# Kernel optimization log

Hardware: AMD Instinct MI355X
Metric: run time of the kernel (lower is better)

The kernel has to match this reference:

```python
import jax, jax.numpy as jnp
import numpy as np

N, M, D, H, T = 8192, 8192, 64, 32, 8
KERNEL_SCALE = 1.0


def setup_inputs() -> dict:
    key = jax.random.key(0)
    ks = jax.random.split(key, 8)
    s1 = 1.0 / np.sqrt(D)
    s2 = 1.0 / np.sqrt(H)
    return {
        "X": jax.random.normal(ks[0], (N, D), jnp.float32),
        "Y": jax.random.normal(ks[1], (M, D), jnp.float32),
        "Y_target": jax.random.normal(ks[2], (M, T), jnp.float32),
        "W1": jax.random.normal(ks[3], (D, H), jnp.float32) * s1,
        "b1": jnp.zeros((H,), jnp.float32),
        "W2": jax.random.normal(ks[4], (H, H), jnp.float32) * s2,
        "b2": jnp.zeros((H,), jnp.float32),
        "W3": jax.random.normal(ks[5], (H, H), jnp.float32) * s2,
        "b3": jnp.zeros((H,), jnp.float32),
    }


def _mlp(x, W1, b1, W2, b2, W3, b3):
    h = jax.nn.relu(x @ W1 + b1)
    h = jax.nn.relu(h @ W2 + b2)
    return jax.nn.relu(h @ W3 + b3)


def reference(X, Y, Y_target, W1, b1, W2, b2, W3, b3):
    Xf = _mlp(X, W1, b1, W2, b2, W3, b3)  # [N, H]
    Yf = _mlp(Y, W1, b1, W2, b2, W3, b3)  # [M, H]
    sq = (
        jnp.sum(Xf * Xf, axis=1, keepdims=True)
        + jnp.sum(Yf * Yf, axis=1)[None, :]
        - 2.0 * (Xf @ Yf.T)
    )
    sq = jnp.maximum(sq, 0.0)  # guard tiny negatives from cancellation
    kernel = jnp.exp(-sq / (2.0 * KERNEL_SCALE**2))  # [N, M]
    weights = kernel / jnp.sum(kernel, axis=1, keepdims=True)
    return weights @ Y_target  # [N, T]
```

## Files before the change

### kernel.cpp

```cpp
#include <hip/hip_runtime.h>
#include <hip/hip_bf16.h>
#include <cstddef>

#define N_ROWS 8192
#define M_ROWS 8192
#define D_IN   64
#define H_DIM  32
#define T_OUT  8
#define FDIM   48

#define NSPLIT   32
#define JSLICE   (M_ROWS / NSPLIT)
#define JTILE    32
#define NTILES   (JSLICE / JTILE)
#define LOG2E    1.4426950408889634f
#define NHALF_SC (-0.72134752044448169f)

typedef _Float16 half8  __attribute__((ext_vector_type(8)));
typedef _Float16 half4v __attribute__((ext_vector_type(4)));
typedef __fp16   fp16x2 __attribute__((ext_vector_type(2)));
typedef float    f32x16 __attribute__((ext_vector_type(16)));

__device__ __forceinline__ half8 ld_h8(const _Float16* p) {
    return *(const half8*)p;
}


__global__ __launch_bounds__(256) void feat_kernel(
    const float* __restrict__ X, const float* __restrict__ Y,
    const float* __restrict__ W1, const float* __restrict__ b1,
    const float* __restrict__ W2, const float* __restrict__ b2,
    const float* __restrict__ W3, const float* __restrict__ b3,
    _Float16* __restrict__ fh, _Float16* __restrict__ fl)
{
    __shared__ float xs [32 * 65];
    __shared__ float w1l[64 * 36];
    __shared__ float w2l[32 * 36];
    __shared__ float w3l[32 * 36];
    __shared__ float h1t[32 * 33];
    __shared__ float h2t[32 * 33];
    __shared__ float psums[8 * 32];
    __shared__ float bl[96];

    const int tid = threadIdx.x;
    const int rowbase = blockIdx.x * 32;
    const bool isX = rowbase < N_ROWS;
    const float* src = isX ? (X + (size_t)rowbase * D_IN)
                           : (Y + (size_t)(rowbase - N_ROWS) * D_IN);

    {
        const float4* g4 = (const float4*)src;
        int i0 = tid * 2;
        float4 v0 = g4[i0], v1 = g4[i0 + 1];
        int f0 = tid * 8;
        int r = f0 >> 6, c = f0 & 63;
        float* dst = xs + r * 65 + c;
        dst[0] = v0.x; dst[1] = v0.y; dst[2] = v0.z; dst[3] = v0.w;
        dst[4] = v1.x; dst[5] = v1.y; dst[6] = v1.z; dst[7] = v1.w;
    }
    {
        const float4* g4 = (const float4*)W1;
        int i0 = tid * 2;
        float4 v0 = g4[i0], v1 = g4[i0 + 1];
        int f0 = tid * 8;
        int r = f0 >> 5, c = f0 & 31;
        float* dst = w1l + r * 36 + c;
        ((float4*)dst)[0] = v0; ((float4*)dst)[1] = v1;
    }
    {
        int f0 = tid * 4;
        int r = f0 >> 5, c = f0 & 31;
        *(float4*)(w2l + r * 36 + c) = ((const float4*)W2)[tid];
        *(float4*)(w3l + r * 36 + c) = ((const float4*)W3)[tid];
    }
    if (tid < 32) { bl[tid] = b1[tid]; bl[32 + tid] = b2[tid]; bl[64 + tid] = b3[tid]; }
    __syncthreads();

    const int r  = tid & 31;
    const int c0 = (tid >> 5) * 4;

    float4 a1 = *(const float4*)(bl + c0);
    #pragma unroll
    for (int k = 0; k < 64; ++k) {
        float xv = xs[r * 65 + k];
        float4 w = *(const float4*)(w1l + k * 36 + c0);
        a1.x = fmaf(xv, w.x, a1.x);
        a1.y = fmaf(xv, w.y, a1.y);
        a1.z = fmaf(xv, w.z, a1.z);
        a1.w = fmaf(xv, w.w, a1.w);
    }
    h1t[(c0 + 0) * 33 + r] = fmaxf(a1.x, 0.f);
    h1t[(c0 + 1) * 33 + r] = fmaxf(a1.y, 0.f);
    h1t[(c0 + 2) * 33 + r] = fmaxf(a1.z, 0.f);
    h1t[(c0 + 3) * 33 + r] = fmaxf(a1.w, 0.f);
    __syncthreads();

    float4 a2 = *(const float4*)(bl + 32 + c0);
    #pragma unroll
    for (int k = 0; k < 32; ++k) {
        float xv = h1t[k * 33 + r];
        float4 w = *(const float4*)(w2l + k * 36 + c0);
        a2.x = fmaf(xv, w.x, a2.x);
        a2.y = fmaf(xv, w.y, a2.y);
        a2.z = fmaf(xv, w.z, a2.z);
        a2.w = fmaf(xv, w.w, a2.w);
    }
    h2t[(c0 + 0) * 33 + r] = fmaxf(a2.x, 0.f);
    h2t[(c0 + 1) * 33 + r] = fmaxf(a2.y, 0.f);
    h2t[(c0 + 2) * 33 + r] = fmaxf(a2.z, 0.f);
    h2t[(c0 + 3) * 33 + r] = fmaxf(a2.w, 0.f);
    __syncthreads();

    float4 a3 = *(const float4*)(bl + 64 + c0);
    #pragma unroll
    for (int k = 0; k < 32; ++k) {
        float xv = h2t[k * 33 + r];
        float4 w = *(const float4*)(w3l + k * 36 + c0);
        a3.x = fmaf(xv, w.x, a3.x);
        a3.y = fmaf(xv, w.y, a3.y);
        a3.z = fmaf(xv, w.z, a3.z);
        a3.w = fmaf(xv, w.w, a3.w);
    }
    float v0 = fmaxf(a3.x, 0.f), v1 = fmaxf(a3.y, 0.f);
    float v2 = fmaxf(a3.z, 0.f), v3 = fmaxf(a3.w, 0.f);

    psums[(tid >> 5) * 32 + r] = v0 * v0 + v1 * v1 + v2 * v2 + v3 * v3;

    const float scale = isX ? LOG2E : 1.0f;
    union { _Float16 h[4]; uint2 u; } hh, ll;
    float sv0 = v0 * scale, sv1 = v1 * scale, sv2 = v2 * scale, sv3 = v3 * scale;
    hh.h[0] = (_Float16)sv0; hh.h[1] = (_Float16)sv1;
    hh.h[2] = (_Float16)sv2; hh.h[3] = (_Float16)sv3;
    ll.h[0] = (_Float16)(sv0 - (float)hh.h[0]);
    ll.h[1] = (_Float16)(sv1 - (float)hh.h[1]);
    ll.h[2] = (_Float16)(sv2 - (float)hh.h[2]);
    ll.h[3] = (_Float16)(sv3 - (float)hh.h[3]);
    {
        const int tile = blockIdx.x;
        const int ch = c0 >> 4, hb = (c0 >> 3) & 1, off = c0 & 7;
        const size_t fi = (((size_t)(tile * 3 + ch) * 64) + hb * 32 + r) * 8 + off;
        *(uint2*)(fh + fi) = hh.u;
        *(uint2*)(fl + fi) = ll.u;
    }

    __syncthreads();
    if (tid < 32) {
        float nrm = 0.f;
        #pragma unroll
        for (int g = 0; g < 8; ++g) nrm += psums[g * 32 + tid];
        float qn = NHALF_SC * nrm;
        float d32 = isX ? qn : 1.0f;
        float d33 = isX ? 1.0f : qn;
        union { _Float16 h[8]; uint4 q; } eh, el, ez;
        #pragma unroll
        for (int i = 0; i < 8; ++i) { eh.h[i] = (_Float16)0.f; el.h[i] = (_Float16)0.f; ez.h[i] = (_Float16)0.f; }
        _Float16 h32 = (_Float16)d32, h33 = (_Float16)d33;
        eh.h[0] = h32; eh.h[1] = h33;
        el.h[0] = (_Float16)(d32 - (float)h32);
        el.h[1] = (_Float16)(d33 - (float)h33);
        const int tile = blockIdx.x;
        const size_t f0 = (((size_t)(tile * 3 + 2) * 64) + tid) * 8;
        const size_t f1 = (((size_t)(tile * 3 + 2) * 64) + 32 + tid) * 8;
        *(uint4*)(fh + f0) = eh.q;  *(uint4*)(fh + f1) = ez.q;
        *(uint4*)(fl + f0) = el.q;  *(uint4*)(fl + f1) = ez.q;
    }
}

__global__ __launch_bounds__(256) void ytt_kernel(
    const float* __restrict__ Yt,
    _Float16* __restrict__ yfh, _Float16* __restrict__ yfl)
{
    const int idx = blockIdx.x * 256 + threadIdx.x;
    const int lane = idx & 63;
    const int jtg  = idx >> 6;
    const int g    = jtg & 3;
    const int jt   = jtg >> 2;
    const int t    = lane & 31;
    const int h    = lane >> 5;
    const int j    = jt * 32 + g * 8 + h * 4;
    union { _Float16 hh[4]; uint2 u; } H, L;
    #pragma unroll
    for (int i = 0; i < 4; ++i) {
        float v = (t < T_OUT) ? Yt[(size_t)(j + i) * T_OUT + t]
                              : (t == 8 ? 1.0f : 0.0f);
        _Float16 hi = (_Float16)v;
        H.hh[i] = hi;
        L.hh[i] = (_Float16)(v - (float)hi);
    }
    *(uint2*)(yfh + (size_t)idx * 4) = H.u;
    *(uint2*)(yfl + (size_t)idx * 4) = L.u;
}

__global__ __launch_bounds__(256, 4) void pair_kernel(
    const _Float16* __restrict__ fh, const _Float16* __restrict__ fl,
    const _Float16* __restrict__ yfh, const _Float16* __restrict__ yfl,
    float* __restrict__ pout, float* __restrict__ psum)
{
    const int tid  = threadIdx.x;
    const int wave = tid >> 6;
    const int lane = tid & 63;
    const int n    = lane & 31;
    const int h    = lane >> 5;

    const int rowtile = blockIdx.x * 4 + wave;
    const int rowbase = rowtile * 32;
    const int s       = blockIdx.y;

    const size_t qoff = ((size_t)rowtile * 3) * 512 + (size_t)lane * 8;
    half8 qh0 = ld_h8(fh + qoff);
    half8 qh1 = ld_h8(fh + qoff + 512);
    half8 qh2 = ld_h8(fh + qoff + 1024);
    half8 ql0 = ld_h8(fl + qoff);
    half8 ql1 = ld_h8(fl + qoff + 512);
    half8 ql2 = ld_h8(fl + qoff + 1024);

    f32x16 o = {};

    const int ktile0 = (N_ROWS / 32) + s * NTILES;

    for (int jt = 0; jt < NTILES; ++jt) {
        const size_t koff = ((size_t)(ktile0 + jt) * 3) * 512 + (size_t)lane * 8;
        half8 kh0 = ld_h8(fh + koff);
        half8 kh1 = ld_h8(fh + koff + 512);
        half8 kh2 = ld_h8(fh + koff + 1024);
        half8 kl0 = ld_h8(fl + koff);
        half8 kl1 = ld_h8(fl + koff + 512);
        half8 kl2 = ld_h8(fl + koff + 1024);

        f32x16 acc = {};
        acc = __builtin_amdgcn_mfma_f32_32x32x16_f16(kh0, qh0, acc, 0, 0, 0);
        acc = __builtin_amdgcn_mfma_f32_32x32x16_f16(kh1, qh1, acc, 0, 0, 0);
        acc = __builtin_amdgcn_mfma_f32_32x32x16_f16(kh2, qh2, acc, 0, 0, 0);
        acc = __builtin_amdgcn_mfma_f32_32x32x16_f16(kh0, ql0, acc, 0, 0, 0);
        acc = __builtin_amdgcn_mfma_f32_32x32x16_f16(kh1, ql1, acc, 0, 0, 0);
        acc = __builtin_amdgcn_mfma_f32_32x32x16_f16(kh2, ql2, acc, 0, 0, 0);
        acc = __builtin_amdgcn_mfma_f32_32x32x16_f16(kl0, qh0, acc, 0, 0, 0);
        acc = __builtin_amdgcn_mfma_f32_32x32x16_f16(kl1, qh1, acc, 0, 0, 0);
        acc = __builtin_amdgcn_mfma_f32_32x32x16_f16(kl2, qh2, acc, 0, 0, 0);

        half4v phi[4];
        #pragma unroll
        for (int g = 0; g < 4; ++g) {
            float w0 = __builtin_amdgcn_exp2f(fminf(acc[4*g+0], 0.f));
            float w1 = __builtin_amdgcn_exp2f(fminf(acc[4*g+1], 0.f));
            float w2 = __builtin_amdgcn_exp2f(fminf(acc[4*g+2], 0.f));
            float w3 = __builtin_amdgcn_exp2f(fminf(acc[4*g+3], 0.f));
            fp16x2 p01 = __builtin_amdgcn_cvt_pkrtz(w0, w1);
            fp16x2 p23 = __builtin_amdgcn_cvt_pkrtz(w2, w3);
            union { unsigned int u[2]; half4v v; } ph;
            ph.u[0] = __builtin_bit_cast(unsigned int, p01);
            ph.u[1] = __builtin_bit_cast(unsigned int, p23);
            phi[g] = ph.v;
        }

        const size_t yb = ((size_t)((s * NTILES + jt) * 4) * 64 + lane) * 4;
        #pragma unroll
        for (int g = 0; g < 4; ++g) {
            half4v bh = *(const half4v*)(yfh + yb + (size_t)g * 256);
            half4v bv = *(const half4v*)(yfl + yb + (size_t)g * 256);
            o = __builtin_amdgcn_mfma_f32_32x32x8f16(phi[g], bh, o, 0, 0, 0);
            o = __builtin_amdgcn_mfma_f32_32x32x8f16(phi[g], bv, o, 0, 0, 0);
        }
    }

    const int t = n;
    if (t <= 8) {
        #pragma unroll
        for (int r = 0; r < 16; ++r) {
            int i = (r & 3) + 8 * (r >> 2) + 4 * h;
            int row = rowbase + i;
            float v = o[r];
            if (t < 8)
                pout[((size_t)s * N_ROWS + row) * T_OUT + t] = v;
            else
                psum[(size_t)s * N_ROWS + row] = v;
        }
    }
}

__global__ __launch_bounds__(256) void reduce_kernel(
    const float* __restrict__ pout, const float* __restrict__ psum,
    float* __restrict__ out)
{
    const int id = blockIdx.x * 256 + threadIdx.x;
    const int i = id >> 3;
    float sv = 0.f, sw = 0.f;
    #pragma unroll
    for (int s = 0; s < NSPLIT; ++s) {
        sv += pout[(size_t)s * N_ROWS * T_OUT + id];
        sw += psum[(size_t)s * N_ROWS + i];
    }
    out[id] = sv / sw;
}

extern "C" void kernel_launch(void* const* d_in, const int* in_sizes, int n_in,
                              void* d_out, int out_size, void* d_ws, size_t ws_size,
                              hipStream_t stream)
{
    const float* X  = (const float*)d_in[0];
    const float* Y  = (const float*)d_in[1];
    const float* Yt = (const float*)d_in[2];
    const float* W1 = (const float*)d_in[3];
    const float* b1 = (const float*)d_in[4];
    const float* W2 = (const float*)d_in[5];
    const float* b2 = (const float*)d_in[6];
    const float* W3 = (const float*)d_in[7];
    const float* b3 = (const float*)d_in[8];
    float* out = (float*)d_out;

    char* ws = (char*)d_ws;
    const size_t n_feat = (size_t)((N_ROWS + M_ROWS) / 32) * 3 * 512;
    _Float16* fh  = (_Float16*)ws;   ws += n_feat * 2;
    _Float16* fl  = (_Float16*)ws;   ws += n_feat * 2;
    const size_t n_yf = (size_t)(M_ROWS / JTILE) * 4 * 64 * 4;
    _Float16* yfh = (_Float16*)ws;   ws += n_yf * 2;
    _Float16* yfl = (_Float16*)ws;   ws += n_yf * 2;
    float*    pout = (float*)ws;     ws += (size_t)NSPLIT * N_ROWS * T_OUT * 4;
    float*    psum = (float*)ws;

    feat_kernel<<<(N_ROWS + M_ROWS) / 32, 256, 0, stream>>>(
        X, Y, W1, b1, W2, b2, W3, b3, fh, fl);
    ytt_kernel<<<(M_ROWS / JTILE) * 4 * 64 / 256, 256, 0, stream>>>(Yt, yfh, yfl);

    dim3 grid2(N_ROWS / 128, NSPLIT);
    pair_kernel<<<grid2, 256, 0, stream>>>(fh, fl, yfh, yfl, pout, psum);

    reduce_kernel<<<(N_ROWS * T_OUT) / 256, 256, 0, stream>>>(pout, psum, out);
}
```

Measured before the change: 121.2 us.

## Stage key and target tiles through double-buffered LDS with async global-to-LDS loads

The pair kernel now loads each iteration's key-feature and target tiles once per block into shared memory using global_load_lds. This replaces having each of the four waves fetch the same tiles from global memory. Two buffers alternate, so the next tile is prefetched while the current one feeds the MFMA and exp work. The aim is to remove redundant global/L2 traffic and hide load latency. In exchange it adds a block-wide barrier every iteration and 20 KB of LDS per block, on a loop of only eight iterations.

```diff
diff --git a/kernel.cpp b/kernel.cpp
--- a/kernel.cpp
+++ b/kernel.cpp
@@ -15,6 +15,12 @@
 #define NTILES   (JSLICE / JTILE)
 #define LOG2E    1.4426950408889634f
 #define NHALF_SC (-0.72134752044448169f)
+
+#define KH_OFF 0
+#define KL_OFF 3072
+#define YH_OFF 6144
+#define YL_OFF 8192
+#define BUFSZ  10240
 
 typedef _Float16 half8  __attribute__((ext_vector_type(8)));
 typedef _Float16 half4v __attribute__((ext_vector_type(4)));
@@ -196,6 +202,8 @@
     const _Float16* __restrict__ yfh, const _Float16* __restrict__ yfl,
     float* __restrict__ pout, float* __restrict__ psum)
 {
+    __shared__ char smem[2 * BUFSZ];
+
     const int tid  = threadIdx.x;
     const int wave = tid >> 6;
     const int lane = tid & 63;
@@ -205,8 +213,9 @@
     const int rowtile = blockIdx.x * 4 + wave;
     const int rowbase = rowtile * 32;
     const int s       = blockIdx.y;
-
-    const size_t qoff = ((size_t)rowtile * 3) * 512 + (size_t)lane * 8;
+    const int ktile0  = (N_ROWS / 32) + s * NTILES;
+
+    const size_t qoff = (size_t)rowtile * 1536 + (size_t)lane * 8;
     half8 qh0 = ld_h8(fh + qoff);
     half8 qh1 = ld_h8(fh + qoff + 512);
     half8 qh2 = ld_h8(fh + qoff + 1024);
@@ -214,18 +223,42 @@
     half8 ql1 = ld_h8(fl + qoff + 512);
     half8 ql2 = ld_h8(fl + qoff + 1024);
 
+    auto prefetch = [&](int jt, char* buf) {
+        const char* srcKh = (const char*)(fh + (size_t)(ktile0 + jt) * 1536);
+        const char* srcKl = (const char*)(fl + (size_t)(ktile0 + jt) * 1536);
+        const char* srcYh = (const char*)(yfh + (size_t)(s * NTILES + jt) * 1024);
+        const char* srcYl = (const char*)(yfl + (size_t)(s * NTILES + jt) * 1024);
+        #pragma unroll
+        for (int r = 0; r < 3; ++r) {
+            const int c0 = wave * 64 + r * 256;
+            const int c  = c0 + lane;
+            const char* g; char* l;
+            if (c0 < 192)      { g = srcKh + (size_t)c * 16;         l = buf + KH_OFF + c * 16; }
+            else if (c0 < 384) { g = srcKl + (size_t)(c - 192) * 16; l = buf + KL_OFF + (c - 192) * 16; }
+            else if (c0 < 512) { g = srcYh + (size_t)(c - 384) * 16; l = buf + YH_OFF + (c - 384) * 16; }
+            else if (c0 < 640) { g = srcYl + (size_t)(c - 512) * 16; l = buf + YL_OFF + (c - 512) * 16; }
+            else break;
+            __builtin_amdgcn_global_load_lds(
+                (const __attribute__((address_space(1))) void*)g,
+                (__attribute__((address_space(3))) void*)l, 16, 0, 0);
+        }
+    };
+
     f32x16 o = {};
 
-    const int ktile0 = (N_ROWS / 32) + s * NTILES;
+    prefetch(0, smem);
+    __syncthreads();
 
     for (int jt = 0; jt < NTILES; ++jt) {
-        const size_t koff = ((size_t)(ktile0 + jt) * 3) * 512 + (size_t)lane * 8;
-        half8 kh0 = ld_h8(fh + koff);
-        half8 kh1 = ld_h8(fh + koff + 512);
-        half8 kh2 = ld_h8(fh + koff + 1024);
-        half8 kl0 = ld_h8(fl + koff);
-        half8 kl1 = ld_h8(fl + koff + 512);
-        half8 kl2 = ld_h8(fl + koff + 1024);
+        char* cur = smem + (jt & 1) * BUFSZ;
+        if (jt + 1 < NTILES) prefetch(jt + 1, smem + ((jt + 1) & 1) * BUFSZ);
+
+        half8 kh0 = *(const half8*)(cur + KH_OFF + lane * 16);
+        half8 kh1 = *(const half8*)(cur + KH_OFF + 1024 + lane * 16);
+        half8 kh2 = *(const half8*)(cur + KH_OFF + 2048 + lane * 16);
+        half8 kl0 = *(const half8*)(cur + KL_OFF + lane * 16);
+        half8 kl1 = *(const half8*)(cur + KL_OFF + 1024 + lane * 16);
+        half8 kl2 = *(const half8*)(cur + KL_OFF + 2048 + lane * 16);
 
         f32x16 acc = {};
         acc = __builtin_amdgcn_mfma_f32_32x32x16_f16(kh0, qh0, acc, 0, 0, 0);
@@ -253,14 +286,15 @@
             phi[g] = ph.v;
         }
 
-        const size_t yb = ((size_t)((s * NTILES + jt) * 4) * 64 + lane) * 4;
         #pragma unroll
         for (int g = 0; g < 4; ++g) {
-            half4v bh = *(const half4v*)(yfh + yb + (size_t)g * 256);
-            half4v bv = *(const half4v*)(yfl + yb + (size_t)g * 256);
+            half4v bh = *(const half4v*)(cur + YH_OFF + (g * 64 + lane) * 8);
+            half4v bv = *(const half4v*)(cur + YL_OFF + (g * 64 + lane) * 8);
             o = __builtin_amdgcn_mfma_f32_32x32x8f16(phi[g], bh, o, 0, 0, 0);
             o = __builtin_amdgcn_mfma_f32_32x32x8f16(phi[g], bv, o, 0, 0, 0);
         }
+
+        __syncthreads();
     }
 
     const int t = n;
```

New measurement: 112.6 us. 7.1% less time.

## Stage key tiles in LDS with async double buffering and drop norm-augmented MFMA chunk

Applied to the files above, without the earlier changes.

The pair kernel now stages two key tiles and their Y_target fragments into a double-buffered LDS region using global_load_lds, so the next stage's loads overlap the current stage's MFMAs. The squared-norm terms are no longer folded into a third augmented feature chunk. They are stored as separate floats and added before exp2, which cuts the QK MFMAs from 9 to 6 per tile. The two prep kernels are merged into one launch, Y_target hi/lo are interleaved into a single buffer, and NSPLIT is halved so fewer partial sums are written. The cost is extra LDS use and a barrier per stage, which may limit occupancy, plus fewer blocks in flight.

```diff
diff --git a/kernel.cpp b/kernel.cpp
--- a/kernel.cpp
+++ b/kernel.cpp
@@ -7,14 +7,18 @@
 #define D_IN   64
 #define H_DIM  32
 #define T_OUT  8
-#define FDIM   48
-
-#define NSPLIT   32
+
+#define NSPLIT   16
 #define JSLICE   (M_ROWS / NSPLIT)
 #define JTILE    32
 #define NTILES   (JSLICE / JTILE)
+#define NSTAGES  (NTILES / 2)
 #define LOG2E    1.4426950408889634f
 #define NHALF_SC (-0.72134752044448169f)
+
+#define YI_OFF  8192
+#define CK_OFF  16384
+#define STAGEBUF 16640
 
 typedef _Float16 half8  __attribute__((ext_vector_type(8)));
 typedef _Float16 half4v __attribute__((ext_vector_type(4)));
@@ -26,12 +30,14 @@
 }
 
 
-__global__ __launch_bounds__(256) void feat_kernel(
+__global__ __launch_bounds__(256) void prep_kernel(
     const float* __restrict__ X, const float* __restrict__ Y,
+    const float* __restrict__ Yt,
     const float* __restrict__ W1, const float* __restrict__ b1,
     const float* __restrict__ W2, const float* __restrict__ b2,
     const float* __restrict__ W3, const float* __restrict__ b3,
-    _Float16* __restrict__ fh, _Float16* __restrict__ fl)
+    _Float16* __restrict__ fh, _Float16* __restrict__ fl,
+    _Float16* __restrict__ yfi, float* __restrict__ ns)
 {
     __shared__ float xs [32 * 65];
     __shared__ float w1l[64 * 36];
@@ -43,6 +49,29 @@
     __shared__ float bl[96];
 
     const int tid = threadIdx.x;
+
+    if (blockIdx.x >= 512) {
+        const int idx = (blockIdx.x - 512) * 256 + tid;
+        const int lane = idx & 63;
+        const int jtg  = idx >> 6;
+        const int g    = jtg & 3;
+        const int jt   = jtg >> 2;
+        const int t    = lane & 31;
+        const int h    = lane >> 5;
+        const int j    = jt * 32 + g * 8 + h * 4;
+        union { _Float16 hh[8]; uint4 u; } V;
+        #pragma unroll
+        for (int i = 0; i < 4; ++i) {
+            float v = (t < T_OUT) ? Yt[(size_t)(j + i) * T_OUT + t]
+                                  : (t == 8 ? 1.0f : 0.0f);
+            _Float16 hi = (_Float16)v;
+            V.hh[i]     = hi;
+            V.hh[4 + i] = (_Float16)(v - (float)hi);
+        }
+        *(uint4*)(yfi + (size_t)idx * 8) = V.u;
+        return;
+    }
+
     const int rowbase = blockIdx.x * 32;
     const bool isX = rowbase < N_ROWS;
     const float* src = isX ? (X + (size_t)rowbase * D_IN)
@@ -138,7 +167,7 @@
     {
         const int tile = blockIdx.x;
         const int ch = c0 >> 4, hb = (c0 >> 3) & 1, off = c0 & 7;
-        const size_t fi = (((size_t)(tile * 3 + ch) * 64) + hb * 32 + r) * 8 + off;
+        const size_t fi = (((size_t)(tile * 2 + ch) * 64) + hb * 32 + r) * 8 + off;
         *(uint2*)(fh + fi) = hh.u;
         *(uint2*)(fl + fi) = ll.u;
     }
@@ -148,54 +177,17 @@
         float nrm = 0.f;
         #pragma unroll
         for (int g = 0; g < 8; ++g) nrm += psums[g * 32 + tid];
-        float qn = NHALF_SC * nrm;
-        float d32 = isX ? qn : 1.0f;
-        float d33 = isX ? 1.0f : qn;
-        union { _Float16 h[8]; uint4 q; } eh, el, ez;
-        #pragma unroll
-        for (int i = 0; i < 8; ++i) { eh.h[i] = (_Float16)0.f; el.h[i] = (_Float16)0.f; ez.h[i] = (_Float16)0.f; }
-        _Float16 h32 = (_Float16)d32, h33 = (_Float16)d33;
-        eh.h[0] = h32; eh.h[1] = h33;
-        el.h[0] = (_Float16)(d32 - (float)h32);
-        el.h[1] = (_Float16)(d33 - (float)h33);
-        const int tile = blockIdx.x;
-        const size_t f0 = (((size_t)(tile * 3 + 2) * 64) + tid) * 8;
-        const size_t f1 = (((size_t)(tile * 3 + 2) * 64) + 32 + tid) * 8;
-        *(uint4*)(fh + f0) = eh.q;  *(uint4*)(fh + f1) = ez.q;
-        *(uint4*)(fl + f0) = el.q;  *(uint4*)(fl + f1) = ez.q;
-    }
-}
-
-__global__ __launch_bounds__(256) void ytt_kernel(
-    const float* __restrict__ Yt,
-    _Float16* __restrict__ yfh, _Float16* __restrict__ yfl)
-{
-    const int idx = blockIdx.x * 256 + threadIdx.x;
-    const int lane = idx & 63;
-    const int jtg  = idx >> 6;
-    const int g    = jtg & 3;
-    const int jt   = jtg >> 2;
-    const int t    = lane & 31;
-    const int h    = lane >> 5;
-    const int j    = jt * 32 + g * 8 + h * 4;
-    union { _Float16 hh[4]; uint2 u; } H, L;
-    #pragma unroll
-    for (int i = 0; i < 4; ++i) {
-        float v = (t < T_OUT) ? Yt[(size_t)(j + i) * T_OUT + t]
-                              : (t == 8 ? 1.0f : 0.0f);
-        _Float16 hi = (_Float16)v;
-        H.hh[i] = hi;
-        L.hh[i] = (_Float16)(v - (float)hi);
-    }
-    *(uint2*)(yfh + (size_t)idx * 4) = H.u;
-    *(uint2*)(yfl + (size_t)idx * 4) = L.u;
+        ns[rowbase + tid] = NHALF_SC * nrm;
+    }
 }
 
 __global__ __launch_bounds__(256, 4) void pair_kernel(
     const _Float16* __restrict__ fh, const _Float16* __restrict__ fl,
-    const _Float16* __restrict__ yfh, const _Float16* __restrict__ yfl,
+    const _Float16* __restrict__ yfi, const float* __restrict__ ns,
     float* __restrict__ pout, float* __restrict__ psum)
 {
+    __shared__ char smem[2 * STAGEBUF];
+
     const int tid  = threadIdx.x;
     const int wave = tid >> 6;
     const int lane = tid & 63;
@@ -205,62 +197,95 @@
     const int rowtile = blockIdx.x * 4 + wave;
     const int rowbase = rowtile * 32;
     const int s       = blockIdx.y;
-
-    const size_t qoff = ((size_t)rowtile * 3) * 512 + (size_t)lane * 8;
+    const int ktile0  = (N_ROWS / 32) + s * NTILES;
+    const int jstart  = s * JSLICE;
+
+    const size_t qoff = (size_t)rowtile * 1024 + (size_t)lane * 8;
     half8 qh0 = ld_h8(fh + qoff);
     half8 qh1 = ld_h8(fh + qoff + 512);
-    half8 qh2 = ld_h8(fh + qoff + 1024);
     half8 ql0 = ld_h8(fl + qoff);
     half8 ql1 = ld_h8(fl + qoff + 512);
-    half8 ql2 = ld_h8(fl + qoff + 1024);
+
+    const float qvn = ns[rowbase + n];
+
+    auto prefetch = [&](int st, char* buf) {
+        const int kt = ktile0 + 2 * st;
+        const char* fhA = (const char*)(fh + (size_t)kt * 1024);
+        const char* flA = (const char*)(fl + (size_t)kt * 1024);
+        const char* fhB = (const char*)(fh + (size_t)(kt + 1) * 1024);
+        const char* flB = (const char*)(fl + (size_t)(kt + 1) * 1024);
+        const char* yA  = (const char*)(yfi + (size_t)(s * NTILES + 2 * st) * 2048);
+        const char* yB  = (const char*)(yfi + (size_t)(s * NTILES + 2 * st + 1) * 2048);
+        #pragma unroll
+        for (int r = 0; r < 4; ++r) {
+            const int c0 = wave * 64 + r * 256;
+            const int c  = c0 + lane;
+            const char* g; char* l;
+            if (c0 < 128)      { g = fhA + (size_t)c * 16;         l = buf + c * 16; }
+            else if (c0 < 256) { g = flA + (size_t)(c - 128) * 16; l = buf + 2048 + (c - 128) * 16; }
+            else if (c0 < 384) { g = fhB + (size_t)(c - 256) * 16; l = buf + 4096 + (c - 256) * 16; }
+            else if (c0 < 512) { g = flB + (size_t)(c - 384) * 16; l = buf + 6144 + (c - 384) * 16; }
+            else if (c0 < 768) { g = yA  + (size_t)(c - 512) * 16; l = buf + YI_OFF + (c - 512) * 16; }
+            else               { g = yB  + (size_t)(c - 768) * 16; l = buf + YI_OFF + 4096 + (c - 768) * 16; }
+            __builtin_amdgcn_global_load_lds(
+                (const __attribute__((address_space(1))) void*)g,
+                (__attribute__((address_space(3))) void*)l, 16, 0, 0);
+        }
+        if (wave == 0) {
+            const char* gc = (const char*)(ns + N_ROWS + jstart + st * 64 + lane);
+            __builtin_amdgcn_global_load_lds(
+                (const __attribute__((address_space(1))) void*)gc,
+                (__attribute__((address_space(3))) void*)(buf + CK_OFF), 4, 0, 0);
+        }
+    };
 
     f32x16 o = {};
 
-    const int ktile0 = (N_ROWS / 32) + s * NTILES;
-
-    for (int jt = 0; jt < NTILES; ++jt) {
-        const size_t koff = ((size_t)(ktile0 + jt) * 3) * 512 + (size_t)lane * 8;
-        half8 kh0 = ld_h8(fh + koff);
-        half8 kh1 = ld_h8(fh + koff + 512);
-        half8 kh2 = ld_h8(fh + koff + 1024);
-        half8 kl0 = ld_h8(fl + koff);
-        half8 kl1 = ld_h8(fl + koff + 512);
-        half8 kl2 = ld_h8(fl + koff + 1024);
+    auto compute = [&](const char* buf, int sub) {
+        const char* kb = buf + sub * 4096;
+        half8 kh0 = *(const half8*)(kb + lane * 16);
+        half8 kh1 = *(const half8*)(kb + 1024 + lane * 16);
+        half8 kl0 = *(const half8*)(kb + 2048 + lane * 16);
+        half8 kl1 = *(const half8*)(kb + 3072 + lane * 16);
 
         f32x16 acc = {};
         acc = __builtin_amdgcn_mfma_f32_32x32x16_f16(kh0, qh0, acc, 0, 0, 0);
         acc = __builtin_amdgcn_mfma_f32_32x32x16_f16(kh1, qh1, acc, 0, 0, 0);
-        acc = __builtin_amdgcn_mfma_f32_32x32x16_f16(kh2, qh2, acc, 0, 0, 0);
         acc = __builtin_amdgcn_mfma_f32_32x32x16_f16(kh0, ql0, acc, 0, 0, 0);
         acc = __builtin_amdgcn_mfma_f32_32x32x16_f16(kh1, ql1, acc, 0, 0, 0);
-        acc = __builtin_amdgcn_mfma_f32_32x32x16_f16(kh2, ql2, acc, 0, 0, 0);
         acc = __builtin_amdgcn_mfma_f32_32x32x16_f16(kl0, qh0, acc, 0, 0, 0);
         acc = __builtin_amdgcn_mfma_f32_32x32x16_f16(kl1, qh1, acc, 0, 0, 0);
-        acc = __builtin_amdgcn_mfma_f32_32x32x16_f16(kl2, qh2, acc, 0, 0, 0);
-
-        half4v phi[4];
+
+        const char* ckb = buf + CK_OFF + sub * 128;
+        const char* yb  = buf + YI_OFF + sub * 4096;
         #pragma unroll
         for (int g = 0; g < 4; ++g) {
-            float w0 = __builtin_amdgcn_exp2f(fminf(acc[4*g+0], 0.f));
-            float w1 = __builtin_amdgcn_exp2f(fminf(acc[4*g+1], 0.f));
-            float w2 = __builtin_amdgcn_exp2f(fminf(acc[4*g+2], 0.f));
-            float w3 = __builtin_amdgcn_exp2f(fminf(acc[4*g+3], 0.f));
-            fp16x2 p01 = __builtin_amdgcn_cvt_pkrtz(w0, w1);
-            fp16x2 p23 = __builtin_amdgcn_cvt_pkrtz(w2, w3);
+            float4 ck4 = *(const float4*)(ckb + (8 * g + 4 * h) * 4);
+            float w0 = __builtin_amdgcn_exp2f(fminf(acc[4*g+0] + (ck4.x + qvn), 0.f));
+            float w1 = __builtin_amdgcn_exp2f(fminf(acc[4*g+1] + (ck4.y + qvn), 0.f));
+            float w2 = __builtin_amdgcn_exp2f(fminf(acc[4*g+2] + (ck4.z + qvn), 0.f));
+            float w3 = __builtin_amdgcn_exp2f(fminf(acc[4*g+3] + (ck4.w + qvn), 0.f));
             union { unsigned int u[2]; half4v v; } ph;
-            ph.u[0] = __builtin_bit_cast(unsigned int, p01);
-            ph.u[1] = __builtin_bit_cast(unsigned int, p23);
-            phi[g] = ph.v;
-        }
-
-        const size_t yb = ((size_t)((s * NTILES + jt) * 4) * 64 + lane) * 4;
-        #pragma unroll
-        for (int g = 0; g < 4; ++g) {
-            half4v bh = *(const half4v*)(yfh + yb + (size_t)g * 256);
-            half4v bv = *(const half4v*)(yfl + yb + (size_t)g * 256);
-            o = __builtin_amdgcn_mfma_f32_32x32x8f16(phi[g], bh, o, 0, 0, 0);
-            o = __builtin_amdgcn_mfma_f32_32x32x8f16(phi[g], bv, o, 0, 0, 0);
-        }
+            ph.u[0] = __builtin_bit_cast(unsigned int, __builtin_amdgcn_cvt_pkrtz(w0, w1));
+            ph.u[1] = __builtin_bit_cast(unsigned int, __builtin_amdgcn_cvt_pkrtz(w2, w3));
+            uint4 yv = *(const uint4*)(yb + (g * 64 + lane) * 16);
+            union { unsigned int u[2]; half4v v; } yh, yl;
+            yh.u[0] = yv.x; yh.u[1] = yv.y;
+            yl.u[0] = yv.z; yl.u[1] = yv.w;
+            o = __builtin_amdgcn_mfma_f32_32x32x8f16(ph.v, yh.v, o, 0, 0, 0);
+            o = __builtin_amdgcn_mfma_f32_32x32x8f16(ph.v, yl.v, o, 0, 0, 0);
+        }
+    };
+
+    prefetch(0, smem);
+    __syncthreads();
+
+    for (int st = 0; st < NSTAGES; ++st) {
+        char* cur = smem + (st & 1) * STAGEBUF;
+        if (st + 1 < NSTAGES) prefetch(st + 1, smem + ((st + 1) & 1) * STAGEBUF);
+        compute(cur, 0);
+        compute(cur, 1);
+        __syncthreads();
     }
 
     const int t = n;
@@ -309,21 +334,20 @@
     float* out = (float*)d_out;
 
     char* ws = (char*)d_ws;
-    const size_t n_feat = (size_t)((N_ROWS + M_ROWS) / 32) * 3 * 512;
+    const size_t n_feat = (size_t)((N_ROWS + M_ROWS) / 32) * 2 * 512;
     _Float16* fh  = (_Float16*)ws;   ws += n_feat * 2;
     _Float16* fl  = (_Float16*)ws;   ws += n_feat * 2;
-    const size_t n_yf = (size_t)(M_ROWS / JTILE) * 4 * 64 * 4;
-    _Float16* yfh = (_Float16*)ws;   ws += n_yf * 2;
-    _Float16* yfl = (_Float16*)ws;   ws += n_yf * 2;
+    const size_t n_yfi = (size_t)(M_ROWS / JTILE) * 4 * 64 * 8;
+    _Float16* yfi = (_Float16*)ws;   ws += n_yfi * 2;
+    float*    ns  = (float*)ws;      ws += (N_ROWS + M_ROWS) * 4;
     float*    pout = (float*)ws;     ws += (size_t)NSPLIT * N_ROWS * T_OUT * 4;
     float*    psum = (float*)ws;
 
-    feat_kernel<<<(N_ROWS + M_ROWS) / 32, 256, 0, stream>>>(
-        X, Y, W1, b1, W2, b2, W3, b3, fh, fl);
-    ytt_kernel<<<(M_ROWS / JTILE) * 4 * 64 / 256, 256, 0, stream>>>(Yt, yfh, yfl);
+    prep_kernel<<<512 + 256, 256, 0, stream>>>(
+        X, Y, Yt, W1, b1, W2, b2, W3, b3, fh, fl, yfi, ns);
 
     dim3 grid2(N_ROWS / 128, NSPLIT);
-    pair_kernel<<<grid2, 256, 0, stream>>>(fh, fl, yfh, yfl, pout, psum);
+    pair_kernel<<<grid2, 256, 0, stream>>>(fh, fl, yfi, ns, pout, psum);
 
     reduce_kernel<<<(N_ROWS * T_OUT) / 256, 256, 0, stream>>>(pout, psum, out);
 }
```

Result: faster. 103.8 us (median of 2 runs) (-14.4%).
